# Kernel optimization log

Measured on AMD Instinct MI355X. Metric: run time of the kernel, lower is better.

## Reference

```python
import jax, jax.numpy as jnp
import numpy as np

D_MODEL = 512
D_FF = 2048
NUM_EXPERTS = 8
TOP_K = 2


def setup_inputs() -> dict:
    key = jax.random.key(0)
    k_x, k_r, k_w1, k_w2 = jax.random.split(key, 4)
    x = jax.random.normal(k_x, (4, 2048, D_MODEL), dtype=jnp.float32)
    # router: Linear(d_model -> num_experts, bias=False); weight [E, D]
    Wr = jax.random.normal(k_r, (NUM_EXPERTS, D_MODEL), dtype=jnp.float32) * (1.0 / np.sqrt(D_MODEL))
    # expert weights: W1 [E, d_ff, d_model], W2 [E, d_model, d_ff] (torch Linear layout)
    W1 = jax.random.normal(k_w1, (NUM_EXPERTS, D_FF, D_MODEL), dtype=jnp.float32) * (1.0 / np.sqrt(D_MODEL))
    W2 = jax.random.normal(k_w2, (NUM_EXPERTS, D_MODEL, D_FF), dtype=jnp.float32) * (1.0 / np.sqrt(D_FF))
    return {"x": x, "Wr": Wr, "W1": W1, "W2": W2}


def reference(x, Wr, W1, W2):
    B, L, D = x.shape
    T = B * L
    x_flat = x.reshape(T, D)

    # Router: logits -> softmax -> top-k -> scatter back to dense [T, E]
    logits = x_flat @ Wr.T  # router_temperature = 1.0
    sm = jax.nn.softmax(logits, axis=-1)
    top_v, top_i = jax.lax.top_k(sm, TOP_K)  # [T, k]
    probs = jnp.zeros_like(sm).at[jnp.arange(T)[:, None], top_i].set(top_v)

    # All-expert FFN (dense, as in the original): h = GELU(x W1^T), y = h W2^T
    h = jnp.einsum('td,efd->tef', x_flat, W1)  # [T, E, d_ff]
    h = jax.nn.gelu(h, approximate=False)      # torch nn.GELU default = exact erf
    expert_out = jnp.einsum('tef,edf->ted', h, W2)  # [T, E, D]

    # Weighted combine over experts (dropout is identity in eval mode)
    out = jnp.einsum('te,ted->td', probs, expert_out)
    return out.reshape(B, L, D)
```

## Files before the change

### kernel.cpp

```cpp
#include <hip/hip_runtime.h>
#include <hip/hip_bf16.h>
#include <math.h>

#define D_MODEL 512
#define D_FF    2048
#define NE      8
#define T_TOK   8192
#define SLABU   (16384 * 64)

typedef __attribute__((ext_vector_type(8))) short bf16x8;
typedef __attribute__((ext_vector_type(4))) float f32x4;

static __device__ __forceinline__ unsigned short f2bf(float f){
    union { float f; unsigned u; } v; v.f = f;
    unsigned r = v.u + 0x7FFFu + ((v.u >> 16) & 1u);
    return (unsigned short)(r >> 16);
}
static __device__ __forceinline__ float bf2f(unsigned short u){
    union { unsigned u; float f; } v; v.u = ((unsigned)u) << 16; return v.f;
}

static __device__ __forceinline__ float gelu_f(float x){
    float z = 0.7978845608028654f * (x + 0.044715f * x * x * x);
    float e = __builtin_amdgcn_exp2f(z * 2.8853900817779268f);
    float t = 1.f - 2.f * __builtin_amdgcn_rcpf(e + 1.f);
    return 0.5f * x * (1.f + t);
}

static __device__ __forceinline__ void gload16(const void* g, void* l){
    __builtin_amdgcn_global_load_lds((const __attribute__((address_space(1))) unsigned int*)g,
                                     (__attribute__((address_space(3))) unsigned int*)l, 16, 0, 0);
}

__global__ __launch_bounds__(256) void cvt2_f32_bf16(const float* __restrict__ s1,
                                                     unsigned short* __restrict__ d1,
                                                     const float* __restrict__ s2,
                                                     unsigned short* __restrict__ d2,
                                                     int n4){
    int i = blockIdx.x * blockDim.x + threadIdx.x;
    int stride = gridDim.x * blockDim.x;
    for (; i < 2 * n4; i += stride){
        const float* s = (i < n4) ? s1 : s2;
        unsigned short* d = (i < n4) ? d1 : d2;
        int j = (i < n4) ? i : i - n4;
        float4 v = ((const float4*)s)[j];
        ushort4 o;
        o.x = f2bf(v.x); o.y = f2bf(v.y); o.z = f2bf(v.z); o.w = f2bf(v.w);
        ((ushort4*)d)[j] = o;
    }
}

__global__ __launch_bounds__(512) void router_kernel(const float* __restrict__ x,
                                                     const float* __restrict__ Wr,
                                                     unsigned short* __restrict__ x_bf,
                                                     float* __restrict__ pair_prob,
                                                     int* __restrict__ lists,
                                                     int* __restrict__ cnt){
    __shared__ int s_ei[128];

    int tid  = threadIdx.x;
    int wv   = tid >> 6;
    int lane = tid & 63;
    int tblk = blockIdx.x * 64;

    #pragma unroll 1
    for (int i = 0; i < 8; ++i){
        int tl = wv * 8 + i;
        int t  = tblk + tl;
        const float* xr = x + (size_t)t * D_MODEL;
        float xv[8];
        #pragma unroll
        for (int c = 0; c < 8; ++c) xv[c] = xr[lane + 64*c];
        unsigned short* xb = x_bf + (size_t)t * D_MODEL;
        #pragma unroll
        for (int c = 0; c < 8; ++c) xb[lane + 64*c] = f2bf(xv[c]);
        float lg[NE];
        #pragma unroll
        for (int e = 0; e < NE; ++e){
            const float* wr = Wr + (size_t)e * D_MODEL;
            float s = 0.f;
            #pragma unroll
            for (int c = 0; c < 8; ++c) s = fmaf(xv[c], wr[lane + 64*c], s);
            #pragma unroll
            for (int off = 32; off; off >>= 1) s += __shfl_xor(s, off);
            lg[e] = s;
        }
        if (lane == 0){
            float m = lg[0];
            #pragma unroll
            for (int e = 1; e < NE; ++e) m = fmaxf(m, lg[e]);
            float sum = 0.f;
            #pragma unroll
            for (int e = 0; e < NE; ++e) sum += expf(lg[e] - m);
            int i0 = 0; float v0 = lg[0];
            #pragma unroll
            for (int e = 1; e < NE; ++e) if (lg[e] > v0){ v0 = lg[e]; i0 = e; }
            int i1 = -1; float v1 = -1e30f;
            #pragma unroll
            for (int e = 0; e < NE; ++e) if (e != i0 && lg[e] > v1){ v1 = lg[e]; i1 = e; }
            float inv = 1.f / sum;
            pair_prob[2*t]   = expf(v0 - m) * inv;
            pair_prob[2*t+1] = expf(v1 - m) * inv;
            s_ei[2*tl]     = i0;
            s_ei[2*tl + 1] = i1;
        }
    }
    __syncthreads();

    if (wv == 0){
        int e0 = s_ei[lane];
        int e1 = s_ei[64 + lane];
        unsigned long long below = (lane == 63) ? ~0ull >> 1 : (1ull << lane) - 1;
        unsigned long long m0[NE];
        int rank0 = 0, rank1 = 0, tot = 0;
        #pragma unroll
        for (int ex = 0; ex < NE; ++ex){
            m0[ex] = __ballot(e0 == ex);
            if (e0 == ex) rank0 = __popcll(m0[ex] & below);
        }
        #pragma unroll
        for (int ex = 0; ex < NE; ++ex){
            unsigned long long m1 = __ballot(e1 == ex);
            if (e1 == ex) rank1 = __popcll(m1 & below) + __popcll(m0[ex]);
            if (lane == ex) tot = __popcll(m0[ex]) + __popcll(m1);
        }
        int base_held = 0;
        if (lane < NE) base_held = atomicAdd(&cnt[lane], tot);
        int b0 = __shfl(base_held, e0);
        int b1 = __shfl(base_held, e1);
        int pairbase = blockIdx.x * 128;
        lists[e0 * T_TOK + b0 + rank0] = pairbase + lane;
        lists[e1 * T_TOK + b1 + rank1] = pairbase + 64 + lane;
    }
}


__global__ __launch_bounds__(256, 4) void gemm1_kernel(const unsigned short* __restrict__ x_bf,
                                                       const unsigned short* __restrict__ W1bf,
                                                       const float* __restrict__ pair_prob,
                                                       const int* __restrict__ lists,
                                                       const int* __restrict__ cnt,
                                                       unsigned short* __restrict__ H){
    __shared__ __align__(16) unsigned char lds_a[16384];
    __shared__ __align__(16) unsigned char lds_b[16384];
    __shared__ int   s_tok[128];
    __shared__ float s_prob[128];

    int bid = blockIdx.x;
    int q = bid >> 7, r = bid & 127;
    int tg = q * 8 + (r & 7);
    int f0 = (r >> 3) << 7;
    int e = -1, tm = 0, rem = tg, pfx = 0;
    for (int i = 0; i < NE; ++i){
        int c = cnt[i];
        int mt = (c + 127) >> 7;
        if (e < 0){ if (rem < mt){ e = i; tm = rem; } else { rem -= mt; pfx += c; } }
    }
    if (e < 0) return;
    int ne = cnt[e];

    int tid = threadIdx.x;
    if (tid < 128){
        int idx = tm * 128 + tid;
        int pair = (idx < ne) ? lists[e * T_TOK + idx] : 0;
        s_tok[tid]  = (idx < ne) ? (pair >> 1) : 0;
        s_prob[tid] = (idx < ne) ? pair_prob[pair] : 0.f;
    }
    __syncthreads();

    int wv = tid >> 6, lane = tid & 63, l15 = lane & 15, lk = lane >> 4;
    int wm = wv >> 1, wn = wv & 1;

    int scol = (((lane & 7) ^ (lane >> 3)) << 3);
    const unsigned short* pa[4];
    const unsigned short* pb[4];
    #pragma unroll
    for (int j = 0; j < 4; ++j){
        int row = j * 32 + wv * 8 + (lane >> 3);
        pa[j] = x_bf + (size_t)s_tok[row] * D_MODEL + scol;
        pb[j] = W1bf + ((size_t)e * D_FF + f0 + row) * D_MODEL + scol;
    }
    int dstoff = wv * 1024;

    f32x4 zero4 = {0.f, 0.f, 0.f, 0.f};
    f32x4 acc[4][4];
    #pragma unroll
    for (int i = 0; i < 4; ++i)
        #pragma unroll
        for (int j = 0; j < 4; ++j) acc[i][j] = zero4;

    #pragma unroll 1
    for (int k = 0; k < 8; ++k){
        #pragma unroll
        for (int j = 0; j < 4; ++j){
            gload16(pa[j] + k * 64, lds_a + dstoff + j * 4096);
            gload16(pb[j] + k * 64, lds_b + dstoff + j * 4096);
        }
        asm volatile("s_waitcnt vmcnt(0)\n\ts_barrier" ::: "memory");
        #pragma unroll
        for (int kk = 0; kk < 2; ++kk){
            int co = (kk * 64 + lk * 16) ^ ((l15 & 7) << 4);
            bf16x8 a[4], b[4];
            #pragma unroll
            for (int mf = 0; mf < 4; ++mf)
                a[mf] = *(const bf16x8*)(lds_a + (wm * 64 + mf * 16 + l15) * 128 + co);
            #pragma unroll
            for (int nf = 0; nf < 4; ++nf)
                b[nf] = *(const bf16x8*)(lds_b + (wn * 64 + nf * 16 + l15) * 128 + co);
            #pragma unroll
            for (int mf = 0; mf < 4; ++mf)
                #pragma unroll
                for (int nf = 0; nf < 4; ++nf)
                    acc[mf][nf] = __builtin_amdgcn_mfma_f32_16x16x32_bf16(a[mf], b[nf], acc[mf][nf], 0, 0, 0);
        }
        asm volatile("s_waitcnt lgkmcnt(0)\n\ts_barrier" ::: "memory");
    }

    {
        unsigned short* hs = H + (size_t)((f0 >> 6) + wn) * SLABU + l15;
        int gbase = pfx + tm * 128;
        #pragma unroll
        for (int mf = 0; mf < 4; ++mf){
            #pragma unroll
            for (int rr = 0; rr < 4; ++rr){
                int trow = wm * 64 + mf * 16 + lk * 4 + rr;
                if (tm * 128 + trow < ne){
                    float p = s_prob[trow];
                    unsigned short* hrow = hs + (size_t)(gbase + trow) * 64;
                    #pragma unroll
                    for (int nf = 0; nf < 4; ++nf)
                        hrow[nf * 16] = f2bf(p * gelu_f(acc[mf][nf][rr]));
                }
            }
        }
    }
}

__global__ __launch_bounds__(256, 4) void gemm2_kernel(const unsigned short* __restrict__ H,
                                                       const unsigned short* __restrict__ W2bf,
                                                       const int* __restrict__ lists,
                                                       const int* __restrict__ cnt,
                                                       unsigned short* __restrict__ ybuf){
    __shared__ __align__(16) unsigned char lds_a[16384];
    __shared__ __align__(16) unsigned char lds_b[16384];
    __shared__ int s_pair[128];

    int bid = blockIdx.x;
    int q = bid >> 5, r = bid & 31;
    int tg = q * 8 + (r & 7);
    int d0 = (r >> 3) << 7;
    int e = -1, tm = 0, rem = tg, pfx = 0;
    for (int i = 0; i < NE; ++i){
        int c = cnt[i];
        int mt = (c + 127) >> 7;
        if (e < 0){ if (rem < mt){ e = i; tm = rem; } else { rem -= mt; pfx += c; } }
    }
    if (e < 0) return;
    int ne = cnt[e];

    int tid = threadIdx.x;
    if (tid < 128){
        int idx = tm * 128 + tid;
        s_pair[tid] = (idx < ne) ? lists[e * T_TOK + idx] : 0;
    }
    __syncthreads();

    int wv = tid >> 6, lane = tid & 63, l15 = lane & 15, lk = lane >> 4;
    int wm = wv >> 1, wn = wv & 1;

    int scol = (((lane & 7) ^ (lane >> 3)) << 3);
    const unsigned short* pa[4];
    const unsigned short* pb[4];
    int gbase = pfx + tm * 128;
    #pragma unroll
    for (int j = 0; j < 4; ++j){
        int row = j * 32 + wv * 8 + (lane >> 3);
        pa[j] = H + (size_t)(gbase + row) * 64 + scol;
        pb[j] = W2bf + ((size_t)e * D_MODEL + d0 + row) * D_FF + scol;
    }
    int dstoff = wv * 1024;

    f32x4 zero4 = {0.f, 0.f, 0.f, 0.f};
    f32x4 acc[4][4];
    #pragma unroll
    for (int i = 0; i < 4; ++i)
        #pragma unroll
        for (int j = 0; j < 4; ++j) acc[i][j] = zero4;

    #pragma unroll 1
    for (int k = 0; k < 32; ++k){
        #pragma unroll
        for (int j = 0; j < 4; ++j){
            gload16(pa[j] + (size_t)k * SLABU, lds_a + dstoff + j * 4096);
            gload16(pb[j] + k * 64,            lds_b + dstoff + j * 4096);
        }
        asm volatile("s_waitcnt vmcnt(0)\n\ts_barrier" ::: "memory");
        #pragma unroll
        for (int kk = 0; kk < 2; ++kk){
            int co = (kk * 64 + lk * 16) ^ ((l15 & 7) << 4);
            bf16x8 a[4], b[4];
            #pragma unroll
            for (int mf = 0; mf < 4; ++mf)
                a[mf] = *(const bf16x8*)(lds_a + (wm * 64 + mf * 16 + l15) * 128 + co);
            #pragma unroll
            for (int nf = 0; nf < 4; ++nf)
                b[nf] = *(const bf16x8*)(lds_b + (wn * 64 + nf * 16 + l15) * 128 + co);
            #pragma unroll
            for (int mf = 0; mf < 4; ++mf)
                #pragma unroll
                for (int nf = 0; nf < 4; ++nf)
                    acc[mf][nf] = __builtin_amdgcn_mfma_f32_16x16x32_bf16(a[mf], b[nf], acc[mf][nf], 0, 0, 0);
        }
        asm volatile("s_waitcnt lgkmcnt(0)\n\ts_barrier" ::: "memory");
    }

    #pragma unroll
    for (int mf = 0; mf < 4; ++mf){
        #pragma unroll
        for (int rr = 0; rr < 4; ++rr){
            int trow = wm * 64 + mf * 16 + lk * 4 + rr;
            int idx  = tm * 128 + trow;
            if (idx < ne){
                unsigned short* yrow = ybuf + (size_t)s_pair[trow] * D_MODEL + d0 + wn * 64 + l15;
                #pragma unroll
                for (int nf = 0; nf < 4; ++nf)
                    yrow[nf * 16] = f2bf(acc[mf][nf][rr]);
            }
        }
    }
}

__global__ __launch_bounds__(256) void combine_kernel(const unsigned short* __restrict__ ybuf,
                                                      float* __restrict__ out){
    int gid  = blockIdx.x * 256 + threadIdx.x;
    int t    = gid >> 6;
    int lane = gid & 63;
    if (t >= T_TOK) return;
    const unsigned short* y0 = ybuf + (size_t)(2 * t) * D_MODEL + lane * 8;
    const unsigned short* y1 = y0 + D_MODEL;
    unsigned short a[8], b[8];
    *(int4*)a = *(const int4*)y0;
    *(int4*)b = *(const int4*)y1;
    float res[8];
    #pragma unroll
    for (int j = 0; j < 8; ++j) res[j] = bf2f(a[j]) + bf2f(b[j]);
    float* orow = out + (size_t)t * D_MODEL + lane * 8;
    *(float4*)(orow)     = *(float4*)(res);
    *(float4*)(orow + 4) = *(float4*)(res + 4);
}

__global__ __launch_bounds__(512, 2) void moe_ffn_fallback(const unsigned short* __restrict__ x_bf,
                                                           const unsigned short* __restrict__ W1bf,
                                                           const unsigned short* __restrict__ W2bf,
                                                           const float* __restrict__ pair_prob,
                                                           const int* __restrict__ lists,
                                                           const int* __restrict__ cnt,
                                                           float* __restrict__ out){
    __shared__ __align__(16) unsigned char lds_x[64 * 1024];
    __shared__ __align__(16) unsigned char lds_h[64 * 256];
    int bid  = blockIdx.x;
    int xcd  = bid & 7, slot = bid >> 3;
    int eA   = xcd >> 1, sA = xcd & 1;
    int eB   = eA + 4;
    int tA   = (cnt[eA] + 63) >> 6;
    int tB   = (cnt[eB] + 63) >> 6;
    int e, sp, tile;
    if (slot < tA)           { e = eA; sp = sA; tile = slot; }
    else if (slot < tA + tB) { e = eB; sp = sA; tile = slot - tA; }
    else return;
    int ne = cnt[e];
    int tid = threadIdx.x;
    {
        int row = tid >> 3;
        int idx = tile * 64 + row;
        int tok = 0;
        if (idx < ne) tok = lists[e * T_TOK + idx] >> 1;
        int seg = (tid & 7) * 64;
        const unsigned short* src = x_bf + (size_t)tok * D_MODEL + seg;
        int sw = (row & 7) << 4;
        #pragma unroll
        for (int g = 0; g < 8; ++g){
            int4 v = *(const int4*)(src + g * 8);
            int col2 = (seg + g * 8) * 2;
            *(int4*)(lds_x + row * 1024 + (col2 ^ sw)) = v;
        }
    }
    __syncthreads();
    int wv = tid >> 6, lane = tid & 63, l15 = lane & 15, lk = lane >> 4;
    int swz = (l15 & 7) << 4;
    f32x4 zero4 = {0.f, 0.f, 0.f, 0.f};
    f32x4 yacc[4][4];
    #pragma unroll
    for (int i = 0; i < 4; ++i)
        #pragma unroll
        for (int j = 0; j < 4; ++j) yacc[i][j] = zero4;
    const unsigned short* w1p0 = W1bf + ((size_t)e * D_FF + sp * 1024 + wv * 16 + l15) * D_MODEL + lk * 8;
    const unsigned short* w2p0 = W2bf + ((size_t)e * D_MODEL + wv * 64 + l15) * D_FF + sp * 1024 + lk * 8;
    for (int fc = 0; fc < 8; ++fc){
        f32x4 hacc[4];
        #pragma unroll
        for (int at = 0; at < 4; ++at) hacc[at] = zero4;
        const unsigned short* w1p = w1p0 + (size_t)(fc * 128) * D_MODEL;
        #pragma unroll
        for (int ks = 0; ks < 16; ++ks){
            bf16x8 bb = *(const bf16x8*)(w1p + ks * 32);
            int col2 = (ks * 32 + lk * 8) * 2;
            #pragma unroll
            for (int at = 0; at < 4; ++at){
                bf16x8 a = *(const bf16x8*)(lds_x + (at * 16 + l15) * 1024 + (col2 ^ swz));
                hacc[at] = __builtin_amdgcn_mfma_f32_16x16x32_bf16(a, bb, hacc[at], 0, 0, 0);
            }
        }
        {
            int fl2 = (wv * 16 + l15) * 2;
            #pragma unroll
            for (int at = 0; at < 4; ++at){
                #pragma unroll
                for (int rr = 0; rr < 4; ++rr){
                    int tok = at * 16 + lk * 4 + rr;
                    *(unsigned short*)(lds_h + tok * 256 + (fl2 ^ ((tok & 7) << 4))) = f2bf(gelu_f(hacc[at][rr]));
                }
            }
        }
        asm volatile("s_waitcnt lgkmcnt(0)\n\ts_barrier" ::: "memory");
        const unsigned short* w2p = w2p0 + fc * 128;
        #pragma unroll
        for (int ks2 = 0; ks2 < 4; ++ks2){
            int col2 = (ks2 * 32 + lk * 8) * 2;
            bf16x8 am[4];
            #pragma unroll
            for (int mt = 0; mt < 4; ++mt)
                am[mt] = *(const bf16x8*)(lds_h + (mt * 16 + l15) * 256 + (col2 ^ swz));
            #pragma unroll
            for (int nt = 0; nt < 4; ++nt){
                bf16x8 bb = *(const bf16x8*)(w2p + (size_t)nt * 16 * D_FF + ks2 * 32);
                #pragma unroll
                for (int mt = 0; mt < 4; ++mt)
                    yacc[mt][nt] = __builtin_amdgcn_mfma_f32_16x16x32_bf16(am[mt], bb, yacc[mt][nt], 0, 0, 0);
            }
        }
        asm volatile("s_waitcnt lgkmcnt(0)\n\ts_barrier" ::: "memory");
    }
    const int* lrow = lists + e * T_TOK + tile * 64;
    #pragma unroll
    for (int mt = 0; mt < 4; ++mt){
        #pragma unroll
        for (int rr = 0; rr < 4; ++rr){
            int trow = mt * 16 + lk * 4 + rr;
            int idx  = tile * 64 + trow;
            if (idx < ne){
                int pair = lrow[trow];
                float p  = pair_prob[pair];
                float* orow = out + (size_t)(pair >> 1) * D_MODEL;
                #pragma unroll
                for (int nt = 0; nt < 4; ++nt)
                    atomicAdd(orow + wv * 64 + nt * 16 + l15, p * yacc[mt][nt][rr]);
            }
        }
    }
}

extern "C" void kernel_launch(void* const* d_in, const int* in_sizes, int n_in,
                              void* d_out, int out_size, void* d_ws, size_t ws_size,
                              hipStream_t stream){
    const float* x  = (const float*)d_in[0];
    const float* Wr = (const float*)d_in[1];
    const float* W1 = (const float*)d_in[2];
    const float* W2 = (const float*)d_in[3];
    float* out = (float*)d_out;

    char* ws = (char*)d_ws;
    unsigned short* x_bf = (unsigned short*)(ws);
    unsigned short* W1bf = (unsigned short*)(ws + 8388608);
    unsigned short* W2bf = (unsigned short*)(ws + 25165824);
    unsigned short* H    = (unsigned short*)(ws + 41943040);
    float* pair_prob     = (float*)(ws + 109051904);
    int*   lists         = (int*)(ws + 109117440);
    int*   cnt           = (int*)(ws + 109379584);
    unsigned short* ybuf = (unsigned short*)(ws);
    const size_t NEED = 109379616;
    bool big = ws_size >= NEED;
    if (!big){
        pair_prob = (float*)(ws + 41943040);
        lists     = (int*)(ws + 42008576);
        cnt       = (int*)(ws + 42270720);
    }

    hipMemsetAsync(cnt, 0, NE * sizeof(int), stream);

    cvt2_f32_bf16<<<2048, 256, 0, stream>>>(W1, W1bf, W2, W2bf, (NE * D_FF * D_MODEL) / 4);

    router_kernel<<<T_TOK / 64, 512, 0, stream>>>(x, Wr, x_bf, pair_prob, lists, cnt);

    if (big){
        gemm1_kernel<<<17 * 128, 256, 0, stream>>>(x_bf, W1bf, pair_prob, lists, cnt, H);
        gemm2_kernel<<<17 * 32, 256, 0, stream>>>(H, W2bf, lists, cnt, ybuf);
        combine_kernel<<<(T_TOK * 64) / 256, 256, 0, stream>>>(ybuf, out);
    } else {
        hipMemsetAsync(d_out, 0, (size_t)out_size * sizeof(float), stream);
        moe_ffn_fallback<<<2080, 512, 0, stream>>>(x_bf, W1bf, W2bf, pair_prob, lists, cnt, out);
    }
}
```

Before: 143.1 us.

## Load weight fragments directly from global into registers, bypassing LDS

Both grouped GEMM kernels now read the B (weight) operand straight from global memory into per-lane MFMA fragment registers, so the weight LDS buffer and its LDS reads are gone. Only the gathered activation tile is still staged through shared memory. This halves LDS traffic and footprint. In exchange, each weight element is reloaded by both wm warps with less coalesced 16-byte loads, and more registers are used, so launch bounds drop from 4 to 3 blocks per CU.

```diff
diff --git a/kernel.cpp b/kernel.cpp
--- a/kernel.cpp
+++ b/kernel.cpp
@@ -135,14 +135,13 @@
 }
 
 
-__global__ __launch_bounds__(256, 4) void gemm1_kernel(const unsigned short* __restrict__ x_bf,
+__global__ __launch_bounds__(256, 3) void gemm1_kernel(const unsigned short* __restrict__ x_bf,
                                                        const unsigned short* __restrict__ W1bf,
                                                        const float* __restrict__ pair_prob,
                                                        const int* __restrict__ lists,
                                                        const int* __restrict__ cnt,
                                                        unsigned short* __restrict__ H){
     __shared__ __align__(16) unsigned char lds_a[16384];
-    __shared__ __align__(16) unsigned char lds_b[16384];
     __shared__ int   s_tok[128];
     __shared__ float s_prob[128];
 
@@ -173,13 +172,15 @@
 
     int scol = (((lane & 7) ^ (lane >> 3)) << 3);
     const unsigned short* pa[4];
-    const unsigned short* pb[4];
     #pragma unroll
     for (int j = 0; j < 4; ++j){
         int row = j * 32 + wv * 8 + (lane >> 3);
         pa[j] = x_bf + (size_t)s_tok[row] * D_MODEL + scol;
-        pb[j] = W1bf + ((size_t)e * D_FF + f0 + row) * D_MODEL + scol;
-    }
+    }
+    const unsigned short* pbB[4];
+    #pragma unroll
+    for (int nf = 0; nf < 4; ++nf)
+        pbB[nf] = W1bf + ((size_t)e * D_FF + f0 + wn * 64 + nf * 16 + l15) * D_MODEL + lk * 8;
     int dstoff = wv * 1024;
 
     f32x4 zero4 = {0.f, 0.f, 0.f, 0.f};
@@ -191,27 +192,28 @@
 
     #pragma unroll 1
     for (int k = 0; k < 8; ++k){
-        #pragma unroll
-        for (int j = 0; j < 4; ++j){
+        bf16x8 b0[4], b1[4];
+        #pragma unroll
+        for (int nf = 0; nf < 4; ++nf){
+            b0[nf] = *(const bf16x8*)(pbB[nf] + k * 64);
+            b1[nf] = *(const bf16x8*)(pbB[nf] + k * 64 + 32);
+        }
+        #pragma unroll
+        for (int j = 0; j < 4; ++j)
             gload16(pa[j] + k * 64, lds_a + dstoff + j * 4096);
-            gload16(pb[j] + k * 64, lds_b + dstoff + j * 4096);
-        }
         asm volatile("s_waitcnt vmcnt(0)\n\ts_barrier" ::: "memory");
         #pragma unroll
         for (int kk = 0; kk < 2; ++kk){
             int co = (kk * 64 + lk * 16) ^ ((l15 & 7) << 4);
-            bf16x8 a[4], b[4];
+            bf16x8 a[4];
             #pragma unroll
             for (int mf = 0; mf < 4; ++mf)
                 a[mf] = *(const bf16x8*)(lds_a + (wm * 64 + mf * 16 + l15) * 128 + co);
-            #pragma unroll
-            for (int nf = 0; nf < 4; ++nf)
-                b[nf] = *(const bf16x8*)(lds_b + (wn * 64 + nf * 16 + l15) * 128 + co);
             #pragma unroll
             for (int mf = 0; mf < 4; ++mf)
                 #pragma unroll
                 for (int nf = 0; nf < 4; ++nf)
-                    acc[mf][nf] = __builtin_amdgcn_mfma_f32_16x16x32_bf16(a[mf], b[nf], acc[mf][nf], 0, 0, 0);
+                    acc[mf][nf] = __builtin_amdgcn_mfma_f32_16x16x32_bf16(a[mf], kk ? b1[nf] : b0[nf], acc[mf][nf], 0, 0, 0);
         }
         asm volatile("s_waitcnt lgkmcnt(0)\n\ts_barrier" ::: "memory");
     }
@@ -236,13 +238,12 @@
     }
 }
 
-__global__ __launch_bounds__(256, 4) void gemm2_kernel(const unsigned short* __restrict__ H,
+__global__ __launch_bounds__(256, 3) void gemm2_kernel(const unsigned short* __restrict__ H,
                                                        const unsigned short* __restrict__ W2bf,
                                                        const int* __restrict__ lists,
                                                        const int* __restrict__ cnt,
                                                        unsigned short* __restrict__ ybuf){
     __shared__ __align__(16) unsigned char lds_a[16384];
-    __shared__ __align__(16) unsigned char lds_b[16384];
     __shared__ int s_pair[128];
 
     int bid = blockIdx.x;
@@ -270,14 +271,16 @@
 
     int scol = (((lane & 7) ^ (lane >> 3)) << 3);
     const unsigned short* pa[4];
-    const unsigned short* pb[4];
     int gbase = pfx + tm * 128;
     #pragma unroll
     for (int j = 0; j < 4; ++j){
         int row = j * 32 + wv * 8 + (lane >> 3);
         pa[j] = H + (size_t)(gbase + row) * 64 + scol;
-        pb[j] = W2bf + ((size_t)e * D_MODEL + d0 + row) * D_FF + scol;
-    }
+    }
+    const unsigned short* pbB[4];
+    #pragma unroll
+    for (int nf = 0; nf < 4; ++nf)
+        pbB[nf] = W2bf + ((size_t)e * D_MODEL + d0 + wn * 64 + nf * 16 + l15) * D_FF + lk * 8;
     int dstoff = wv * 1024;
 
     f32x4 zero4 = {0.f, 0.f, 0.f, 0.f};
@@ -289,27 +292,28 @@
 
     #pragma unroll 1
     for (int k = 0; k < 32; ++k){
-        #pragma unroll
-        for (int j = 0; j < 4; ++j){
+        bf16x8 b0[4], b1[4];
+        #pragma unroll
+        for (int nf = 0; nf < 4; ++nf){
+            b0[nf] = *(const bf16x8*)(pbB[nf] + k * 64);
+            b1[nf] = *(const bf16x8*)(pbB[nf] + k * 64 + 32);
+        }
+        #pragma unroll
+        for (int j = 0; j < 4; ++j)
             gload16(pa[j] + (size_t)k * SLABU, lds_a + dstoff + j * 4096);
-            gload16(pb[j] + k * 64,            lds_b + dstoff + j * 4096);
-        }
         asm volatile("s_waitcnt vmcnt(0)\n\ts_barrier" ::: "memory");
         #pragma unroll
         for (int kk = 0; kk < 2; ++kk){
             int co = (kk * 64 + lk * 16) ^ ((l15 & 7) << 4);
-            bf16x8 a[4], b[4];
+            bf16x8 a[4];
             #pragma unroll
             for (int mf = 0; mf < 4; ++mf)
                 a[mf] = *(const bf16x8*)(lds_a + (wm * 64 + mf * 16 + l15) * 128 + co);
-            #pragma unroll
-            for (int nf = 0; nf < 4; ++nf)
-                b[nf] = *(const bf16x8*)(lds_b + (wn * 64 + nf * 16 + l15) * 128 + co);
             #pragma unroll
             for (int mf = 0; mf < 4; ++mf)
                 #pragma unroll
                 for (int nf = 0; nf < 4; ++nf)
-                    acc[mf][nf] = __builtin_amdgcn_mfma_f32_16x16x32_bf16(a[mf], b[nf], acc[mf][nf], 0, 0, 0);
+                    acc[mf][nf] = __builtin_amdgcn_mfma_f32_16x16x32_bf16(a[mf], kk ? b1[nf] : b0[nf], acc[mf][nf], 0, 0, 0);
         }
         asm volatile("s_waitcnt lgkmcnt(0)\n\ts_barrier" ::: "memory");
     }
```

After: 257.6 us. 1.8x slower.

## Enlarge gemm1 tiles to 256x256 with double-buffered, phased LDS pipeline

Applied to the files above, without the earlier changes.

gemm1 moves from 128x128 tiles with 4 waves to 256x256 tiles with 8 waves, each wave owning a 32-column strip across all 256 rows. LDS is double-buffered, and global loads for the next K-step are interleaved with four MFMA phases, using partial vmcnt waits and s_setprio. The aim is to hide load latency and raise operand reuse per byte loaded. In exchange it uses more LDS and registers per block, which limits occupancy to 2 blocks per CU, and padding waste grows because per-expert token counts are rounded up to 256.

```diff
diff --git a/kernel.cpp b/kernel.cpp
--- a/kernel.cpp
+++ b/kernel.cpp
@@ -134,102 +134,128 @@
     }
 }
 
-
-__global__ __launch_bounds__(256, 4) void gemm1_kernel(const unsigned short* __restrict__ x_bf,
+__global__ __launch_bounds__(512, 2) void gemm1_kernel(const unsigned short* __restrict__ x_bf,
                                                        const unsigned short* __restrict__ W1bf,
                                                        const float* __restrict__ pair_prob,
                                                        const int* __restrict__ lists,
                                                        const int* __restrict__ cnt,
                                                        unsigned short* __restrict__ H){
-    __shared__ __align__(16) unsigned char lds_a[16384];
-    __shared__ __align__(16) unsigned char lds_b[16384];
-    __shared__ int   s_tok[128];
-    __shared__ float s_prob[128];
+    __shared__ __align__(16) unsigned char lds_a[2][32768];
+    __shared__ __align__(16) unsigned char lds_b[2][32768];
+    __shared__ int   s_tok[256];
+    __shared__ float s_prob[256];
 
     int bid = blockIdx.x;
-    int q = bid >> 7, r = bid & 127;
+    int q = bid >> 6, r = bid & 63;
     int tg = q * 8 + (r & 7);
-    int f0 = (r >> 3) << 7;
+    int f0 = (r >> 3) << 8;
     int e = -1, tm = 0, rem = tg, pfx = 0;
     for (int i = 0; i < NE; ++i){
         int c = cnt[i];
-        int mt = (c + 127) >> 7;
+        int mt = (c + 255) >> 8;
         if (e < 0){ if (rem < mt){ e = i; tm = rem; } else { rem -= mt; pfx += c; } }
     }
     if (e < 0) return;
     int ne = cnt[e];
 
     int tid = threadIdx.x;
-    if (tid < 128){
-        int idx = tm * 128 + tid;
+    if (tid < 256){
+        int idx = tm * 256 + tid;
         int pair = (idx < ne) ? lists[e * T_TOK + idx] : 0;
         s_tok[tid]  = (idx < ne) ? (pair >> 1) : 0;
         s_prob[tid] = (idx < ne) ? pair_prob[pair] : 0.f;
     }
     __syncthreads();
 
-    int wv = tid >> 6, lane = tid & 63, l15 = lane & 15, lk = lane >> 4;
-    int wm = wv >> 1, wn = wv & 1;
-
-    int scol = (((lane & 7) ^ (lane >> 3)) << 3);
+    int wid = tid >> 6, lane = tid & 63, l15 = lane & 15, lk = lane >> 4;
+    int wc  = wid;
+
+    int scol = (((tid & 7) ^ ((tid >> 3) & 7)) << 3);
     const unsigned short* pa[4];
     const unsigned short* pb[4];
     #pragma unroll
     for (int j = 0; j < 4; ++j){
-        int row = j * 32 + wv * 8 + (lane >> 3);
+        int row = j * 64 + (tid >> 3);
         pa[j] = x_bf + (size_t)s_tok[row] * D_MODEL + scol;
         pb[j] = W1bf + ((size_t)e * D_FF + f0 + row) * D_MODEL + scol;
     }
-    int dstoff = wv * 1024;
 
     f32x4 zero4 = {0.f, 0.f, 0.f, 0.f};
-    f32x4 acc[4][4];
-    #pragma unroll
-    for (int i = 0; i < 4; ++i)
-        #pragma unroll
-        for (int j = 0; j < 4; ++j) acc[i][j] = zero4;
+    f32x4 acc[16][2];
+    #pragma unroll
+    for (int i = 0; i < 16; ++i){ acc[i][0] = zero4; acc[i][1] = zero4; }
+    bf16x8 bfrag[2][2];
+
+    #define STG_A(tau, half) { \
+        unsigned char* d_ = lds_a[(tau) & 1] + (half) * 16384 + wid * 1024; \
+        gload16(pa[(half)*2]     + (size_t)(tau) * 64, d_); \
+        gload16(pa[(half)*2 + 1] + (size_t)(tau) * 64, d_ + 8192); }
+    #define STG_B(tau, half) { \
+        unsigned char* d_ = lds_b[(tau) & 1] + (half) * 16384 + wid * 1024; \
+        gload16(pb[(half)*2]     + (size_t)(tau) * 64, d_); \
+        gload16(pb[(half)*2 + 1] + (size_t)(tau) * 64, d_ + 8192); }
+
+    #define PHASE_BODY(J) { \
+        const unsigned char* la_ = lds_a[t & 1]; \
+        bf16x8 a_[4][2]; \
+        _Pragma("unroll") \
+        for (int fr = 0; fr < 4; ++fr) \
+            _Pragma("unroll") \
+            for (int kk = 0; kk < 2; ++kk) \
+                a_[fr][kk] = *(const bf16x8*)(la_ + ((J)*64 + fr*16 + l15) * 128 + ((kk*64 + lk*16) ^ ((l15 & 7) << 4))); \
+        __builtin_amdgcn_s_setprio(1); \
+        _Pragma("unroll") \
+        for (int fr = 0; fr < 4; ++fr) \
+            _Pragma("unroll") \
+            for (int n = 0; n < 2; ++n) \
+                _Pragma("unroll") \
+                for (int kk = 0; kk < 2; ++kk) \
+                    acc[(J)*4 + fr][n] = __builtin_amdgcn_mfma_f32_16x16x32_bf16(a_[fr][kk], bfrag[n][kk], acc[(J)*4 + fr][n], 0, 0, 0); \
+        __builtin_amdgcn_s_setprio(0); \
+        asm volatile("s_barrier" ::: "memory"); }
+
+    STG_B(0, 0); STG_B(0, 1); STG_A(0, 0); STG_A(0, 1); STG_B(1, 0); STG_B(1, 1);
 
     #pragma unroll 1
-    for (int k = 0; k < 8; ++k){
-        #pragma unroll
-        for (int j = 0; j < 4; ++j){
-            gload16(pa[j] + k * 64, lds_a + dstoff + j * 4096);
-            gload16(pb[j] + k * 64, lds_b + dstoff + j * 4096);
-        }
-        asm volatile("s_waitcnt vmcnt(0)\n\ts_barrier" ::: "memory");
-        #pragma unroll
-        for (int kk = 0; kk < 2; ++kk){
-            int co = (kk * 64 + lk * 16) ^ ((l15 & 7) << 4);
-            bf16x8 a[4], b[4];
-            #pragma unroll
-            for (int mf = 0; mf < 4; ++mf)
-                a[mf] = *(const bf16x8*)(lds_a + (wm * 64 + mf * 16 + l15) * 128 + co);
-            #pragma unroll
-            for (int nf = 0; nf < 4; ++nf)
-                b[nf] = *(const bf16x8*)(lds_b + (wn * 64 + nf * 16 + l15) * 128 + co);
-            #pragma unroll
-            for (int mf = 0; mf < 4; ++mf)
+    for (int t = 0; t < 8; ++t){
+        if (t + 1 < 8) STG_A(t + 1, 0);
+        if (t < 7) asm volatile("s_waitcnt vmcnt(6)" ::: "memory");
+        else       asm volatile("s_waitcnt vmcnt(0)" ::: "memory");
+        asm volatile("s_barrier" ::: "memory");
+        {
+            const unsigned char* lb_ = lds_b[t & 1];
+            #pragma unroll
+            for (int n = 0; n < 2; ++n)
                 #pragma unroll
-                for (int nf = 0; nf < 4; ++nf)
-                    acc[mf][nf] = __builtin_amdgcn_mfma_f32_16x16x32_bf16(a[mf], b[nf], acc[mf][nf], 0, 0, 0);
-        }
-        asm volatile("s_waitcnt lgkmcnt(0)\n\ts_barrier" ::: "memory");
-    }
+                for (int kk = 0; kk < 2; ++kk)
+                    bfrag[n][kk] = *(const bf16x8*)(lb_ + (wc*32 + n*16 + l15) * 128 + ((kk*64 + lk*16) ^ ((l15 & 7) << 4)));
+        }
+        PHASE_BODY(0)
+        if (t + 1 < 8) STG_A(t + 1, 1);
+        PHASE_BODY(1)
+        if (t + 2 < 8) STG_B(t + 2, 0);
+        PHASE_BODY(2)
+        if (t + 2 < 8) STG_B(t + 2, 1);
+        PHASE_BODY(3)
+    }
+    #undef STG_A
+    #undef STG_B
+    #undef PHASE_BODY
 
     {
-        unsigned short* hs = H + (size_t)((f0 >> 6) + wn) * SLABU + l15;
-        int gbase = pfx + tm * 128;
-        #pragma unroll
-        for (int mf = 0; mf < 4; ++mf){
+        int gbase = pfx + tm * 256;
+        int slab  = (f0 >> 6) + (wc >> 1);
+        int cbase = (wc & 1) * 32 + l15;
+        #pragma unroll
+        for (int fr = 0; fr < 16; ++fr){
             #pragma unroll
             for (int rr = 0; rr < 4; ++rr){
-                int trow = wm * 64 + mf * 16 + lk * 4 + rr;
-                if (tm * 128 + trow < ne){
+                int trow = fr * 16 + lk * 4 + rr;
+                if (tm * 256 + trow < ne){
                     float p = s_prob[trow];
-                    unsigned short* hrow = hs + (size_t)(gbase + trow) * 64;
-                    #pragma unroll
-                    for (int nf = 0; nf < 4; ++nf)
-                        hrow[nf * 16] = f2bf(p * gelu_f(acc[mf][nf][rr]));
+                    unsigned short* hrow = H + (size_t)slab * SLABU + (size_t)(gbase + trow) * 64 + cbase;
+                    hrow[0]  = f2bf(p * gelu_f(acc[fr][0][rr]));
+                    hrow[16] = f2bf(p * gelu_f(acc[fr][1][rr]));
                 }
             }
         }
@@ -493,7 +519,7 @@
     router_kernel<<<T_TOK / 64, 512, 0, stream>>>(x, Wr, x_bf, pair_prob, lists, cnt);
 
     if (big){
-        gemm1_kernel<<<17 * 128, 256, 0, stream>>>(x_bf, W1bf, pair_prob, lists, cnt, H);
+        gemm1_kernel<<<9 * 64, 512, 0, stream>>>(x_bf, W1bf, pair_prob, lists, cnt, H);
         gemm2_kernel<<<17 * 32, 256, 0, stream>>>(H, W2bf, lists, cnt, ybuf);
         combine_kernel<<<(T_TOK * 64) / 256, 256, 0, stream>>>(ybuf, out);
     } else {
```

New measurement: 176.6 us. +23.4%, slower.
